# Kernel tuning notes

Measured on AMD Instinct MI355X. Metric: run time of the kernel, lower is better.

## Reference

```python
import jax, jax.numpy as jnp
import numpy as np
from jax.scipy.special import logsumexp

WORD_DIM = 512
SCRF_DIM = 256
N_TAGS = 12
ALLOWED_SPAN = 8
START_ID = 10
STOP_ID = 11
SEQ_LEN = 768
N_SPANS = 96


def _compute_scores(h, Wl, bl, Wr, br, Gl, bgl, Gr, bgr, Wt, bt, transitions):
    # h: [1, L, D] already projected by Dense
    Lc, D = h.shape[1], h.shape[2]
    scores = jnp.zeros((1, Lc, Lc, D), h.dtype)
    diag = jnp.arange(Lc)
    ht = h
    scores = scores.at[:, diag, diag].set(ht)
    for sl in range(1, min(ALLOWED_SPAN, Lc)):
        l, r = ht[:, :-1], ht[:, 1:]
        h_hat = 4.0 * jax.nn.sigmoid(l @ Wl.T + bl + r @ Wr.T + br) - 2.0
        # exp/normalize over 3 gates == softmax over gate axis
        g = (l @ Gl.T + bgl + r @ Gr.T + bgr).reshape(1, Lc - sl, 3, D)
        wgt = jax.nn.softmax(g, axis=2)
        ht = wgt[:, :, 0] * h_hat + wgt[:, :, 1] * l + wgt[:, :, 2] * r
        scores = scores.at[:, diag[:Lc - sl], diag[sl:]].set(ht)
    tagsc = scores @ Wt.T + bt  # [1, L, L, T]
    # final[b,i,j,prev,tag] = tagsc[b,i,j,tag] + transitions[prev,tag]
    return tagsc[:, :, :, None, :] + transitions[None, None, None]


def _forward_pass(s5):
    # s5: [1, L, L, T, T]; semi-Markov forward algorithm, windows of width <= ALLOWED_SPAN
    Lc, T = s5.shape[1], s5.shape[3]
    A = ALLOWED_SPAN
    i0 = jnp.arange(1, Lc + 1)
    k = jnp.arange(A)
    p = i0[:, None] - A + k[None, :]              # candidate span-start positions [L, A]
    m = p >= 0                                    # valid window mask (istarts = max(0, i-A))
    x = s5[0][jnp.clip(p, 0), (i0 - 1)[:, None]]  # [L, A, T, T] span scores ending at i-1
    buf0 = jnp.full((A, T), -10000.0, s5.dtype).at[A - 1, START_ID].set(0.0)

    def step(buf, inp):
        xi, mi = inp
        # tmp[k, prev, tag] = score + logalpha[start, prev]
        tmp = jnp.where(mi[:, None, None], xi + buf[:, :, None], -1e30)
        na = logsumexp(tmp, axis=(0, 1))  # [T]
        return jnp.concatenate([buf[1:], na[None]], axis=0), na

    _, alphas = jax.lax.scan(step, buf0, (x, m))
    return alphas[-1, :STOP_ID].sum()


def _gold_score(s5, tags):
    Lc, T = s5.shape[1], s5.shape[3]
    gf = tags[:, :, 0] * (Lc * T * T) + tags[:, :, 1] * (T * T) + tags[:, :, 2] * T + tags[:, :, 3]
    return jnp.take_along_axis(s5.reshape(1, -1), gf, axis=1).sum()


def setup_inputs() -> dict:
    key = jax.random.key(0)
    ks = jax.random.split(key, 16)
    D, W3 = SCRF_DIM, 3 * SCRF_DIM
    s = 0.05
    def w(k, shape):
        return jax.random.normal(k, shape, dtype=jnp.float32) * s
    return {
        "feats": jax.random.normal(ks[0], (1, SEQ_LEN, WORD_DIM), dtype=jnp.float32),
        "tags": jax.random.randint(ks[1], (1, N_SPANS, 4), 0, N_TAGS),
        "Wd": w(ks[2], (D, WORD_DIM)), "bd": jnp.zeros((D,), jnp.float32),
        "Wl": w(ks[3], (D, D)), "bl": jnp.zeros((D,), jnp.float32),
        "Wr": w(ks[4], (D, D)), "br": jnp.zeros((D,), jnp.float32),
        "Gl": w(ks[5], (W3, D)), "bgl": jnp.zeros((W3,), jnp.float32),
        "Gr": w(ks[6], (W3, D)), "bgr": jnp.zeros((W3,), jnp.float32),
        "Wt": w(ks[7], (N_TAGS, D)), "bt": jnp.zeros((N_TAGS,), jnp.float32),
        "transitions": w(ks[8], (N_TAGS, N_TAGS)),
    }


def reference(feats, tags, Wd, bd, Wl, bl, Wr, br, Gl, bgl, Gr, bgr, Wt, bt, transitions):
    h = feats @ Wd.T + bd  # Dense: word_dim -> scrf_dim
    s5 = _compute_scores(h, Wl, bl, Wr, br, Gl, bgl, Gr, bgr, Wt, bt, transitions)
    gold = _gold_score(s5, tags)
    logZ = _forward_pass(s5)
    return logZ - gold
```

## Files before the change

kernel.cpp:

```cpp
#include <hip/hip_runtime.h>

typedef __attribute__((ext_vector_type(8))) short short8;
typedef __attribute__((ext_vector_type(4))) float f32x4;

#define TPAD 100

__device__ __forceinline__ float bf2f(short s) {
  return __uint_as_float(((unsigned)(unsigned short)s) << 16);
}
__device__ __forceinline__ unsigned short f2bf(float f) {
  unsigned u = __float_as_uint(f);
  unsigned rounding = 0x7fffu + ((u >> 16) & 1u);
  return (unsigned short)((u + rounding) >> 16);
}

struct F8 { float4 a, b; };
__device__ __forceinline__ F8 ldf8(const float* p) {
  F8 r; r.a = *(const float4*)p; r.b = *(const float4*)(p + 4); return r;
}
__device__ __forceinline__ short8 cvtF8(F8 v) {
  short8 r;
  r[0]=(short)f2bf(v.a.x); r[1]=(short)f2bf(v.a.y); r[2]=(short)f2bf(v.a.z); r[3]=(short)f2bf(v.a.w);
  r[4]=(short)f2bf(v.b.x); r[5]=(short)f2bf(v.b.y); r[6]=(short)f2bf(v.b.z); r[7]=(short)f2bf(v.b.w);
  return r;
}

__device__ __forceinline__ void stg_f32(float* p, float v) {
  asm volatile("global_store_dword %0, %1, off sc1" :: "v"(p), "v"(v) : "memory");
}
__device__ __forceinline__ void stg_u16(unsigned short* p, unsigned short v) {
  unsigned w = v;
  asm volatile("global_store_short %0, %1, off sc1" :: "v"(p), "v"(w) : "memory");
}
__device__ __forceinline__ void stg_u32(unsigned* p, unsigned v) {
  asm volatile("global_store_dword %0, %1, off sc1" :: "v"(p), "v"(v) : "memory");
}

#define NFLAGS 30688
__device__ __forceinline__ void flag_spin(unsigned* f, unsigned tgt) {
  unsigned n = 0;
  while (__hip_atomic_load(f, __ATOMIC_RELAXED, __HIP_MEMORY_SCOPE_AGENT) < tgt) {
    __builtin_amdgcn_s_sleep(1);
    if (++n > 2000000u) break;
  }
}
#define DRAIN() asm volatile("s_waitcnt vmcnt(0) lgkmcnt(0)" ::: "memory")
#define KTBAR() do { \
  asm volatile("s_waitcnt lgkmcnt(0)" ::: "memory"); \
  __builtin_amdgcn_s_barrier(); \
  __builtin_amdgcn_sched_barrier(0); \
} while (0)

union __align__(16) SmemU {
  struct { unsigned short As[2][64][72]; unsigned short Ws[2][64][72]; float Cs[64][64]; } g;
  struct { unsigned short As8[8][64][72]; float Cs[64][64]; } gi;
  struct { unsigned short rows[8][264]; float sred[96]; float smu; } bn;
  struct { float Bs[96 * TPAD]; float Acs[96 * TPAD]; float red[8]; } t;
  struct { float Qs[2][96 * TPAD]; float vv[4][96]; float red[8]; float redm[4]; } f;
};

__global__ void prep_kernel(const float* __restrict__ bl, const float* __restrict__ br,
                            const float* __restrict__ bgl, const float* __restrict__ bgr,
                            float* __restrict__ bc, unsigned* __restrict__ flags)
{
  int idx = blockIdx.x * 256 + threadIdx.x;
  if (idx < 1024) {
    bc[idx] = (idx < 256) ? bl[idx] + br[idx] : bgl[idx-256] + bgr[idx-256];
  } else {
    int j = idx - 1024;
    if (j < NFLAGS) flags[j] = 0u;
  }
}

__device__ __forceinline__ void treelevel(SmemU& sm,
    const float* Tin, const float* Cin, float* Tout, float* Cout)
{
  const int bid = blockIdx.x;
  const int tid = threadIdx.x;
  const int wv = tid >> 6, lane = tid & 63;
  const int j = bid >> 1;
  const int cs = (bid & 1) * 48;
  const float* Ag = Tin + (size_t)(2*j) * 9216;
  const float* Bg = Tin + (size_t)(2*j + 1) * 9216;

  float4 av[9], bv[9];
  const float* ap = Ag + tid * 36;
  const float* bp = Bg + tid * 36;
  #pragma unroll
  for (int q = 0; q < 9; ++q) av[q] = *(const float4*)(ap + q*4);
  #pragma unroll
  for (int q = 0; q < 9; ++q) bv[q] = *(const float4*)(bp + q*4);
  float ma = 0.f, mb = 0.f;
  #pragma unroll
  for (int q = 0; q < 9; ++q) {
    ma = fmaxf(ma, fmaxf(fmaxf(av[q].x, av[q].y), fmaxf(av[q].z, av[q].w)));
    mb = fmaxf(mb, fmaxf(fmaxf(bv[q].x, bv[q].y), fmaxf(bv[q].z, bv[q].w)));
  }
  #pragma unroll
  for (int off = 32; off; off >>= 1) {
    ma = fmaxf(ma, __shfl_down(ma, off));
    mb = fmaxf(mb, __shfl_down(mb, off));
  }
  if (lane == 0) { sm.t.red[wv] = ma; sm.t.red[4 + wv] = mb; }
  __syncthreads();
  float fa = fmaxf(fmaxf(sm.t.red[0], sm.t.red[1]), fmaxf(sm.t.red[2], sm.t.red[3]));
  float fb = fmaxf(fmaxf(sm.t.red[4], sm.t.red[5]), fmaxf(sm.t.red[6], sm.t.red[7]));
  float ia = 1.0f / fa, ib = 1.0f / fb;

  #pragma unroll
  for (int q = 0; q < 9; ++q) {
    int e = tid*36 + q*4;
    int r = e / 96, k = e - r*96;
    float4 bb = bv[q];
    bb.x *= ib; bb.y *= ib; bb.z *= ib; bb.w *= ib;
    *(float4*)&sm.t.Bs[r*TPAD + k] = bb;
    float4 aa = av[q];
    sm.t.Acs[(k+0)*TPAD + r] = aa.x * ia;
    sm.t.Acs[(k+1)*TPAD + r] = aa.y * ia;
    sm.t.Acs[(k+2)*TPAD + r] = aa.z * ia;
    sm.t.Acs[(k+3)*TPAD + r] = aa.w * ia;
  }
  __syncthreads();

  int tr = tid >> 4, tc = tid & 15;
  int r0 = tr * 6, c0 = cs + tc * 3;
  float acc[6][3];
  #pragma unroll
  for (int i = 0; i < 6; ++i)
    #pragma unroll
    for (int m = 0; m < 3; ++m) acc[i][m] = 0.f;
  for (int k = 0; k < 96; k += 4) {
    float4 a0 = *(const float4*)&sm.t.Acs[(c0+0)*TPAD + k];
    float4 a1 = *(const float4*)&sm.t.Acs[(c0+1)*TPAD + k];
    float4 a2 = *(const float4*)&sm.t.Acs[(c0+2)*TPAD + k];
    #pragma unroll
    for (int i = 0; i < 6; ++i) {
      float4 b = *(const float4*)&sm.t.Bs[(r0+i)*TPAD + k];
      acc[i][0] += b.x*a0.x + b.y*a0.y + b.z*a0.z + b.w*a0.w;
      acc[i][1] += b.x*a1.x + b.y*a1.y + b.z*a1.z + b.w*a1.w;
      acc[i][2] += b.x*a2.x + b.y*a2.y + b.z*a2.z + b.w*a2.w;
    }
  }
  float* op = Tout + (size_t)j * 9216;
  #pragma unroll
  for (int i = 0; i < 6; ++i)
    #pragma unroll
    for (int m = 0; m < 3; ++m)
      stg_f32(&op[(size_t)(r0+i)*96 + c0 + m], acc[i][m]);
  if ((bid & 1) == 0 && tid == 0)
    stg_f32(&Cout[j], Cin[2*j] + Cin[2*j + 1] + __logf(fa) + __logf(fb));
}

__global__ __launch_bounds__(256, 1) void mega_kernel(
    const float* feats, const float* Wd, const float* bd,
    const float* Wl, const float* Wr, const float* Gl, const float* Gr,
    unsigned short* WcB, const float* bc,
    unsigned short* ht, const float* Wt, const float* bt,
    float* Bband, float* Xn, float* muv, const float* trans,
    const int* tags,
    float* T0, float* T1, float* T2, float* T3, float* T4,
    float* C0, float* C1, float* C2, float* C3, float* C4,
    float* out, unsigned* flags)
{
  __shared__ SmemU sm;
  const int bid = blockIdx.x;
  const int tid = threadIdx.x;
  const int wave = tid >> 6, lane = tid & 63;

  if (bid >= 48) {
    for (int j = (bid - 48)*256 + tid; j < 524288; j += 208*256) {
      int o = j >> 9, k = j & 511;
      float v;
      if (k < 256) v = (o < 256) ? Wl[o*256 + k] : Gl[(o-256)*256 + k];
      else { int k2 = k - 256; v = (o < 256) ? Wr[o*256 + k2] : Gr[(o-256)*256 + k2]; }
      stg_u16(&WcB[j], f2bf(v));
    }
    DRAIN();
    __syncthreads();
    if (tid == 0) atomicAdd(&flags[958*32], 1u);
  }

  if (bid < 192) {
    const int p = bid % 12;
    const int lr = tid >> 3;
    const int c8 = (tid & 7) * 8;
    const int q8 = (lane >> 4) * 8;
    if (bid < 48) {
      const int p0 = p * 64;
      const int n0 = (bid / 12) * 64;
      f32x4 acc[4];
      #pragma unroll
      for (int i = 0; i < 4; ++i)
        #pragma unroll
        for (int j = 0; j < 4; ++j) acc[i][j] = 0.f;
      F8 fa0[2], fa1[2], fw0[2], fw1[2];
      #pragma unroll
      for (int q = 0; q < 2; ++q) {
        int kb = q * 64;
        fa0[q] = ldf8(feats + (size_t)(p0 + lr)*512 + kb + c8);
        fa1[q] = ldf8(feats + (size_t)(p0 + lr + 32)*512 + kb + c8);
        fw0[q] = ldf8(Wd + (size_t)(n0 + lr)*512 + kb + c8);
        fw1[q] = ldf8(Wd + (size_t)(n0 + lr + 32)*512 + kb + c8);
      }
      #pragma unroll
      for (int kt = 0; kt < 8; ++kt) {
        const int sb = kt & 1;
        *(short8*)(&sm.g.As[sb][lr][c8])      = cvtF8(fa0[sb]);
        *(short8*)(&sm.g.As[sb][lr + 32][c8]) = cvtF8(fa1[sb]);
        *(short8*)(&sm.g.Ws[sb][lr][c8])      = cvtF8(fw0[sb]);
        *(short8*)(&sm.g.Ws[sb][lr + 32][c8]) = cvtF8(fw1[sb]);
        if (kt < 6) {
          int kb = (kt + 2) * 64;
          fa0[sb] = ldf8(feats + (size_t)(p0 + lr)*512 + kb + c8);
          fa1[sb] = ldf8(feats + (size_t)(p0 + lr + 32)*512 + kb + c8);
          fw0[sb] = ldf8(Wd + (size_t)(n0 + lr)*512 + kb + c8);
          fw1[sb] = ldf8(Wd + (size_t)(n0 + lr + 32)*512 + kb + c8);
        }
        KTBAR();
        #pragma unroll
        for (int kk = 0; kk < 2; ++kk) {
          short8 bfr = *(const short8*)(&sm.g.Ws[sb][wave*16 + (lane & 15)][kk*32 + q8]);
          #pragma unroll
          for (int mt = 0; mt < 4; ++mt) {
            short8 afr = *(const short8*)(&sm.g.As[sb][mt*16 + (lane & 15)][kk*32 + q8]);
            acc[mt] = __builtin_amdgcn_mfma_f32_16x16x32_bf16(afr, bfr, acc[mt], 0, 0, 0);
          }
        }
        KTBAR();
      }
      int o = n0 + wave*16 + (lane & 15);
      float bias = bd[o];
      #pragma unroll
      for (int mt = 0; mt < 4; ++mt)
        #pragma unroll
        for (int r = 0; r < 4; ++r) {
          int row = p0 + mt*16 + (lane >> 4)*4 + r;
          stg_u16(&ht[row*256 + o], f2bf(acc[mt][r] + bias));
        }
      DRAIN();
      __syncthreads();
      if (tid == 0) atomicAdd(&flags[(0*12 + p)*32], 1u);
    }

    const int p0 = p * 64;
    const int n0i = (bid / 12) * 16;
    if (tid == 0) flag_spin(&flags[958*32], 208u);
    __syncthreads();
    short8 wfrag[16];
    {
      const size_t wrow = (size_t)(wave*256 + n0i + (lane & 15)) * 512;
      #pragma unroll
      for (int kt = 0; kt < 8; ++kt)
        #pragma unroll
        for (int kk = 0; kk < 2; ++kk)
          wfrag[kt*2 + kk] = *(const short8*)(WcB + wrow + kt*64 + kk*32 + q8);
    }
    for (int sl = 1; sl <= 7; ++sl) {
      unsigned tgt = (sl == 1) ? 4u : 16u;
      if (tid == 0) flag_spin(&flags[((sl-1)*12 + p)*32], tgt);
      __syncthreads();
      const unsigned short* htp = ht + (size_t)(sl - 1) * 196608;
      unsigned short* htn = ht + (size_t)sl * 196608;
      const int Mvalid = 768 - sl;
      short8 areg[16];
      #pragma unroll
      for (int kt = 0; kt < 4; ++kt) {
        const int kcol = kt * 64;
        areg[kt*2]     = *(const short8*)(htp + (size_t)(p0 + lr)*256 + kcol + c8);
        areg[kt*2 + 1] = *(const short8*)(htp + (size_t)(p0 + lr + 32)*256 + kcol + c8);
      }
      if (tid == 64 && p < 11) flag_spin(&flags[((sl-1)*12 + p + 1)*32], tgt);
      #pragma unroll
      for (int kt = 0; kt < 4; ++kt) {
        *(short8*)(&sm.gi.As8[kt][lr][c8])      = areg[kt*2];
        *(short8*)(&sm.gi.As8[kt][lr + 32][c8]) = areg[kt*2 + 1];
      }
      __syncthreads();
      #pragma unroll
      for (int kt = 4; kt < 8; ++kt) {
        const int kcol = (kt & 3) * 64;
        int g0 = p0 + lr + 1;      if (g0 > 767) g0 = 767;
        int g1 = p0 + lr + 33;     if (g1 > 767) g1 = 767;
        areg[kt*2]     = *(const short8*)(htp + (size_t)g0*256 + kcol + c8);
        areg[kt*2 + 1] = *(const short8*)(htp + (size_t)g1*256 + kcol + c8);
      }
      #pragma unroll
      for (int kt = 4; kt < 8; ++kt) {
        *(short8*)(&sm.gi.As8[kt][lr][c8])      = areg[kt*2];
        *(short8*)(&sm.gi.As8[kt][lr + 32][c8]) = areg[kt*2 + 1];
      }
      __syncthreads();
      f32x4 acc[4];
      #pragma unroll
      for (int i = 0; i < 4; ++i)
        #pragma unroll
        for (int j = 0; j < 4; ++j) acc[i][j] = 0.f;
      #pragma unroll
      for (int kt = 0; kt < 8; ++kt) {
        #pragma unroll
        for (int kk = 0; kk < 2; ++kk) {
          #pragma unroll
          for (int mt = 0; mt < 4; ++mt) {
            short8 afr = *(const short8*)(&sm.gi.As8[kt][mt*16 + (lane & 15)][kk*32 + q8]);
            acc[mt] = __builtin_amdgcn_mfma_f32_16x16x32_bf16(afr, wfrag[kt*2 + kk], acc[mt], 0, 0, 0);
          }
        }
      }
      #pragma unroll
      for (int mt = 0; mt < 4; ++mt)
        #pragma unroll
        for (int r = 0; r < 4; ++r)
          sm.gi.Cs[mt*16 + (lane >> 4)*4 + r][wave*16 + (lane & 15)] = acc[mt][r];
      __syncthreads();

      {
        int dl = tid & 7;
        int d0 = n0i + dl*2;
        int cc0 = dl*2;
        float bz0 = bc[d0],       bz1 = bc[d0+1];
        float b00 = bc[256 + d0], b01 = bc[256 + d0 + 1];
        float b10 = bc[512 + d0], b11 = bc[512 + d0 + 1];
        float b20 = bc[768 + d0], b21 = bc[768 + d0 + 1];
        for (int pr = tid >> 3; pr < 64; pr += 32) {
          int pw = p0 + pr;
          if (pw >= Mvalid) continue;
          float z0 = sm.gi.Cs[pr][cc0]      + bz0, z1 = sm.gi.Cs[pr][cc0+1]      + bz1;
          float g00 = sm.gi.Cs[pr][16+cc0]  + b00, g01 = sm.gi.Cs[pr][16+cc0+1]  + b01;
          float g10 = sm.gi.Cs[pr][32+cc0]  + b10, g11 = sm.gi.Cs[pr][32+cc0+1]  + b11;
          float g20 = sm.gi.Cs[pr][48+cc0]  + b20, g21 = sm.gi.Cs[pr][48+cc0+1]  + b21;
          unsigned lv = *(const unsigned*)(htp + (size_t)pw*256 + d0);
          unsigned rv = *(const unsigned*)(htp + (size_t)(pw+1)*256 + d0);
          float l0 = bf2f((short)(lv & 0xffff)), l1 = bf2f((short)(lv >> 16));
          float r0v = bf2f((short)(rv & 0xffff)), r1v = bf2f((short)(rv >> 16));
          float hh0 = 4.f / (1.f + __expf(-z0)) - 2.f;
          float hh1 = 4.f / (1.f + __expf(-z1)) - 2.f;
          float mg0 = fmaxf(g00, fmaxf(g10, g20));
          float mg1 = fmaxf(g01, fmaxf(g11, g21));
          float e00 = __expf(g00 - mg0), e10 = __expf(g10 - mg0), e20 = __expf(g20 - mg0);
          float e01 = __expf(g01 - mg1), e11 = __expf(g11 - mg1), e21 = __expf(g21 - mg1);
          float o0 = (e00*hh0 + e10*l0 + e20*r0v) / (e00 + e10 + e20);
          float o1 = (e01*hh1 + e11*l1 + e21*r1v) / (e01 + e11 + e21);
          unsigned pack = (unsigned)f2bf(o0) | ((unsigned)f2bf(o1) << 16);
          stg_u32((unsigned*)(htn + (size_t)pw*256 + d0), pack);
        }
      }
      DRAIN();
      __syncthreads();
      if (tid == 0) atomicAdd(&flags[(sl*12 + p)*32], 1u);
    }
  }

  for (int i1 = bid; i1 < 768; i1 += 256) {
    const int i = i1 + 1;
    if (tid < 2) {
      int rlo = i - 8; if (rlo < 0) rlo = 0;
      int tlo = rlo >> 6, thi = (i - 1) >> 6;
      int tt = (tid == 0) ? tlo : thi;
      flag_spin(&flags[(7*12 + tt)*32], 16u);
    }
    __syncthreads();
    {
      int k = tid >> 5, cc = (tid & 31) * 8;
      int pr = i - 8 + k;
      short8 v;
      if (pr >= 0) {
        int slx = 7 - k;
        v = *(const short8*)(ht + ((size_t)slx*768 + pr)*256 + cc);
      } else {
        #pragma unroll
        for (int j = 0; j < 8; ++j) v[j] = 0;
      }
      *(short8*)(&sm.bn.rows[k][cc]) = v;
    }
    __syncthreads();
    float res = -1e30f;
    if (tid < 96) {
      int t = tid >> 3, k = tid & 7;
      int pr = i - 8 + k;
      if (pr >= 0) {
        float acc = 0.f;
        for (int dch = 0; dch < 256; dch += 8) {
          float4 wa = *(const float4*)(Wt + t*256 + dch);
          float4 wb = *(const float4*)(Wt + t*256 + dch + 4);
          short8 hv = *(const short8*)(&sm.bn.rows[k][dch]);
          acc += wa.x*bf2f(hv[0]) + wa.y*bf2f(hv[1]) + wa.z*bf2f(hv[2]) + wa.w*bf2f(hv[3])
               + wb.x*bf2f(hv[4]) + wb.y*bf2f(hv[5]) + wb.z*bf2f(hv[6]) + wb.w*bf2f(hv[7]);
        }
        res = acc + bt[t];
      }
      stg_f32(&Bband[(size_t)i*96 + tid], res);
      sm.bn.sred[tid] = res;
    }
    __syncthreads();
    if (tid < 32) {
      float m = fmaxf(sm.bn.sred[tid], fmaxf(sm.bn.sred[tid+32], sm.bn.sred[tid+64]));
      #pragma unroll
      for (int off = 16; off; off >>= 1) m = fmaxf(m, __shfl_down(m, off));
      if (tid == 0) { stg_f32(&muv[i], m); sm.bn.smu = m; }
    }
    __syncthreads();
    if (tid < 96) stg_f32(&Xn[(size_t)i*96 + tid], __expf(res - sm.bn.smu));
    DRAIN();
    __syncthreads();
    if (tid == 0) atomicAdd(&flags[(96 + i1)*32], 1u);
  }
  if (bid >= 240) return;

  {
    const int chunk = bid / 5;
    const int bxx = bid % 5;
    if (tid < 16) flag_spin(&flags[(96 + 16*chunk + tid)*32], 1u);
    __syncthreads();
    if (bxx == 0 && tid == 0) stg_f32(&C0[chunk], 0.f);
    const int a = chunk * 16;
    const int g = lane / 12;
    const int t = lane - g * 12;
    const int cidx = bxx * 20 + wave * 5 + g;
    const bool active = (g < 5) && (cidx < 96);
    const int c = active ? cidx : 95;
    const int s = c / 12, tau = c - s * 12;
    float Etc[12];
    #pragma unroll
    for (int jj = 0; jj < 12; ++jj) Etc[jj] = __expf(trans[jj*12 + t]);
    float NA[8], V[8];
    #pragma unroll
    for (int jj = 0; jj < 8; ++jj) { NA[jj] = 0.f; V[jj] = 0.f; }
    #pragma unroll
    for (int jj = 0; jj < 8; ++jj) if (jj == s) {
      NA[jj] = (t == tau) ? 1.f : 0.f;
      V[jj]  = Etc[tau];
    }
    const int gbb = (g * 12) * 4;
    #pragma unroll
    for (int m = 1; m <= 16; ++m) {
      const float* xr = Xn + (size_t)(a + m) * 96 + t * 8;
      float4 x0 = *(const float4*)xr;
      float4 x1 = *(const float4*)(xr + 4);
      float sf = __expf(-muv[a + m]);
      float na = x0.x*V[0] + x0.y*V[1] + x0.z*V[2] + x0.w*V[3]
               + x1.x*V[4] + x1.y*V[5] + x1.z*V[6] + x1.w*V[7];
      int nai = __float_as_int(na);
      float nb[12];
      #pragma unroll
      for (int jj = 0; jj < 12; ++jj)
        nb[jj] = __int_as_float(__builtin_amdgcn_ds_bpermute(gbb + jj*4, nai));
      float pp0 = nb[0]*Etc[0] + nb[1]*Etc[1] + nb[2]*Etc[2]   + nb[3]*Etc[3];
      float pp1 = nb[4]*Etc[4] + nb[5]*Etc[5] + nb[6]*Etc[6]   + nb[7]*Etc[7];
      float pp2 = nb[8]*Etc[8] + nb[9]*Etc[9] + nb[10]*Etc[10] + nb[11]*Etc[11];
      float v = (pp0 + pp1) + pp2;
      #pragma unroll
      for (int kq = 0; kq < 7; ++kq) { NA[kq] = NA[kq+1]*sf; V[kq] = V[kq+1]*sf; }
      NA[7] = na; V[7] = v;
    }
    if (active) {
      float* dst = T0 + (size_t)chunk * 9216 + c;
      #pragma unroll
      for (int jj = 0; jj < 8; ++jj) stg_f32(&dst[(size_t)(jj*12 + t) * 96], NA[jj]);
    }
    DRAIN();
    __syncthreads();
    if (tid == 0) atomicAdd(&flags[(864 + chunk)*32], 1u);
  }
  if (bid >= 48) return;

  {
    int j = bid >> 1;
    if (tid < 2) flag_spin(&flags[(864 + 2*j + tid)*32], 5u);
    __syncthreads();
    treelevel(sm, T0, C0, T1, C1);
    DRAIN(); __syncthreads();
    if (tid == 0) atomicAdd(&flags[(912 + j)*32], 1u);
  }
  if (bid >= 24) return;
  {
    int j = bid >> 1;
    if (tid < 2) flag_spin(&flags[(912 + 2*j + tid)*32], 2u);
    __syncthreads();
    treelevel(sm, T1, C1, T2, C2);
    DRAIN(); __syncthreads();
    if (tid == 0) atomicAdd(&flags[(936 + j)*32], 1u);
  }
  if (bid >= 12) return;
  {
    int j = bid >> 1;
    if (tid < 2) flag_spin(&flags[(936 + 2*j + tid)*32], 2u);
    __syncthreads();
    treelevel(sm, T2, C2, T3, C3);
    DRAIN(); __syncthreads();
    if (tid == 0) atomicAdd(&flags[(948 + j)*32], 1u);
  }
  if (bid >= 6) return;
  {
    int j = bid >> 1;
    if (tid < 2) flag_spin(&flags[(948 + 2*j + tid)*32], 2u);
    __syncthreads();
    treelevel(sm, T3, C3, T4, C4);
    DRAIN(); __syncthreads();
    if (tid == 0) atomicAdd(&flags[(954 + j)*32], 1u);
  }
  if (bid) return;

  {
    if (tid < 3) flag_spin(&flags[(954 + tid)*32], 2u);
    __syncthreads();
    float4 P[9];
    const float* p0p = T4 + tid * 36;
    #pragma unroll
    for (int q = 0; q < 9; ++q) P[q] = *(const float4*)(p0p + q*4);

    float gold = 0.f;
    if (tid < 96) {
      int a = tags[tid*4+0], b = tags[tid*4+1], cc = tags[tid*4+2], d = tags[tid*4+3];
      float v = trans[cc*12 + d];
      int sl = b - a;
      if (sl >= 0 && sl < 8) v += Bband[(size_t)(b+1)*96 + d*8 + (7 - sl)];
      else v += bt[d];
      gold = v;
    }
    float mp = 0.f;
    for (int q = tid; q < 768; q += 256) mp += muv[1 + q];
    #pragma unroll
    for (int off = 32; off; off >>= 1) {
      gold += __shfl_down(gold, off);
      mp   += __shfl_down(mp, off);
    }
    if (lane == 0) { sm.f.red[wave] = gold; sm.f.red[4 + wave] = mp; }

    #pragma unroll
    for (int q = 0; q < 9; ++q) {
      int e = tid*36 + q*4;
      int r = e / 96, k = e - r*96;
      *(float4*)&sm.f.Qs[0][r*TPAD + k] = P[q];
    }
    if (tid < 96) sm.f.vv[0][tid] = (tid == 94) ? 1.f : 0.f;
    __syncthreads();
    float gold_t = sm.f.red[0] + sm.f.red[1] + sm.f.red[2] + sm.f.red[3];
    float musum  = sm.f.red[4] + sm.f.red[5] + sm.f.red[6] + sm.f.red[7];
    float Ct = C4[0] + C4[1] + C4[2];

    #pragma unroll
    for (int s = 0; s < 3; ++s) {
      if (s < 2) {
        const float* pn = T4 + (size_t)(s+1)*9216 + tid*36;
        #pragma unroll
        for (int q = 0; q < 9; ++q) P[q] = *(const float4*)(pn + q*4);
      }
      float acc = 0.f;
      if (tid < 96) {
        const float* Qr = &sm.f.Qs[s & 1][tid * TPAD];
        #pragma unroll
        for (int k = 0; k < 96; k += 4) {
          float4 qv = *(const float4*)(Qr + k);
          float4 zv = *(const float4*)&sm.f.vv[s][k];
          acc += qv.x*zv.x + qv.y*zv.y + qv.z*zv.z + qv.w*zv.w;
        }
      }
      float am = (tid < 96) ? acc : 0.f;
      #pragma unroll
      for (int off = 32; off; off >>= 1) am = fmaxf(am, __shfl_down(am, off));
      if (lane == 0) sm.f.redm[wave] = am;
      __syncthreads();
      float mx = fmaxf(fmaxf(sm.f.redm[0], sm.f.redm[1]), fmaxf(sm.f.redm[2], sm.f.redm[3]));
      Ct += __logf(mx);
      if (tid < 96) sm.f.vv[s+1][tid] = acc / mx;
      if (s < 2) {
        #pragma unroll
        for (int q = 0; q < 9; ++q) {
          int e = tid*36 + q*4;
          int r = e / 96, k = e - r*96;
          *(float4*)&sm.f.Qs[(s+1)&1][r*TPAD + k] = P[q];
        }
      }
      __syncthreads();
    }
    if (tid == 0) {
      float lsum = 0.f;
      #pragma unroll
      for (int t = 0; t < 11; ++t) lsum += __logf(sm.f.vv[3][84 + t]);
      out[0] = lsum + 11.f * (Ct + musum) - gold_t;
    }
  }
}

extern "C" void kernel_launch(void* const* d_in, const int* in_sizes, int n_in,
                              void* d_out, int out_size, void* d_ws, size_t ws_size,
                              hipStream_t stream)
{
  const float* feats = (const float*)d_in[0];
  const int*   tags  = (const int*)  d_in[1];
  const float* Wd    = (const float*)d_in[2];
  const float* bd    = (const float*)d_in[3];
  const float* Wl    = (const float*)d_in[4];
  const float* bl    = (const float*)d_in[5];
  const float* Wr    = (const float*)d_in[6];
  const float* br    = (const float*)d_in[7];
  const float* Gl    = (const float*)d_in[8];
  const float* bgl   = (const float*)d_in[9];
  const float* Gr    = (const float*)d_in[10];
  const float* bgr   = (const float*)d_in[11];
  const float* Wt    = (const float*)d_in[12];
  const float* bt    = (const float*)d_in[13];
  const float* trans = (const float*)d_in[14];
  float* out = (float*)d_out;

  char* ws = (char*)d_ws;
  unsigned short* WcB    = (unsigned short*)(ws + 1048576);
  float*          bc     = (float*)         (ws + 2097152);
  unsigned short* ht     = (unsigned short*)(ws + 2101248);
  float*          Bband  = (float*)         (ws + 5246976);
  float*          Xn     = (float*)         (ws + 5542272);
  float*          muv    = (float*)         (ws + 5837568);
  float*          T0     = (float*)         (ws + 5841664);
  float*          T1     = (float*)         (ws + 7611136);
  float*          T2     = (float*)         (ws + 8495872);
  float*          T3     = (float*)         (ws + 8938240);
  float*          T4     = (float*)         (ws + 9159424);
  float*          C0     = (float*)         (ws + 9270016);
  float*          C1     = (float*)         (ws + 9270272);
  float*          C2     = (float*)         (ws + 9270528);
  float*          C3     = (float*)         (ws + 9270784);
  float*          C4     = (float*)         (ws + 9271040);
  unsigned*       flags  = (unsigned*)      (ws + 9271296);

  prep_kernel<<<124, 256, 0, stream>>>(bl, br, bgl, bgr, bc, flags);
  mega_kernel<<<256, 256, 0, stream>>>(feats, Wd, bd, Wl, Wr, Gl, Gr, WcB, bc,
                                       ht, Wt, bt, Bband, Xn, muv, trans, tags,
                                       T0, T1, T2, T3, T4, C0, C1, C2, C3, C4,
                                       out, flags);
}
```

Before: 193.0 us.

## Fuse tree reduction levels into radix-4 steps and drop bf16 weight prepass

The log-space matrix-product tree over forward-pass transfer matrices now combines four matrices per block per level instead of two, cutting the reduction from four flag-synchronised levels to two. Each block chains three 96x96 matmuls in shared memory with double-buffered partial products. Separately, the global bf16 conversion of the combined Wl/Wr/Gl/Gr weights, and the flag wait on it, is removed; each block now converts its own weight fragments from fp32 directly into registers. This trades extra serial matmul work per block, and redundant fp32 weight reads, for fewer grid-wide syncs and a shorter critical path.

```diff
diff --git a/kernel.cpp b/kernel.cpp
--- a/kernel.cpp
+++ b/kernel.cpp
@@ -55,7 +55,7 @@
   struct { unsigned short As[2][64][72]; unsigned short Ws[2][64][72]; float Cs[64][64]; } g;
   struct { unsigned short As8[8][64][72]; float Cs[64][64]; } gi;
   struct { unsigned short rows[8][264]; float sred[96]; float smu; } bn;
-  struct { float Bs[96 * TPAD]; float Acs[96 * TPAD]; float red[8]; } t;
+  struct { float Ms[96 * TPAD]; float Pc[2][96 * TPAD]; float red[8]; } t4;
   struct { float Qs[2][96 * TPAD]; float vv[4][96]; float red[8]; float redm[4]; } f;
 };
 
@@ -72,73 +72,83 @@
   }
 }
 
-__device__ __forceinline__ void treelevel(SmemU& sm,
-    const float* Tin, const float* Cin, float* Tout, float* Cout)
+__device__ __forceinline__ void tree4(SmemU& sm,
+    const float* Tin, const float* Cin, float* Tout, float* Cout, int j, int cs)
 {
-  const int bid = blockIdx.x;
   const int tid = threadIdx.x;
   const int wv = tid >> 6, lane = tid & 63;
-  const int j = bid >> 1;
-  const int cs = (bid & 1) * 48;
-  const float* Ag = Tin + (size_t)(2*j) * 9216;
-  const float* Bg = Tin + (size_t)(2*j + 1) * 9216;
-
-  float4 av[9], bv[9];
-  const float* ap = Ag + tid * 36;
-  const float* bp = Bg + tid * 36;
+  const int tr = tid >> 4, tc = tid & 15;
+  const int r0 = tr * 6, c0 = tc * 3;
+  float logsum = Cin[4*j] + Cin[4*j+1] + Cin[4*j+2] + Cin[4*j+3];
+  float acc[6][3];
+  int cur = 0;
   #pragma unroll
-  for (int q = 0; q < 9; ++q) av[q] = *(const float4*)(ap + q*4);
-  #pragma unroll
-  for (int q = 0; q < 9; ++q) bv[q] = *(const float4*)(bp + q*4);
-  float ma = 0.f, mb = 0.f;
-  #pragma unroll
-  for (int q = 0; q < 9; ++q) {
-    ma = fmaxf(ma, fmaxf(fmaxf(av[q].x, av[q].y), fmaxf(av[q].z, av[q].w)));
-    mb = fmaxf(mb, fmaxf(fmaxf(bv[q].x, bv[q].y), fmaxf(bv[q].z, bv[q].w)));
-  }
-  #pragma unroll
-  for (int off = 32; off; off >>= 1) {
-    ma = fmaxf(ma, __shfl_down(ma, off));
-    mb = fmaxf(mb, __shfl_down(mb, off));
-  }
-  if (lane == 0) { sm.t.red[wv] = ma; sm.t.red[4 + wv] = mb; }
-  __syncthreads();
-  float fa = fmaxf(fmaxf(sm.t.red[0], sm.t.red[1]), fmaxf(sm.t.red[2], sm.t.red[3]));
-  float fb = fmaxf(fmaxf(sm.t.red[4], sm.t.red[5]), fmaxf(sm.t.red[6], sm.t.red[7]));
-  float ia = 1.0f / fa, ib = 1.0f / fb;
-
-  #pragma unroll
-  for (int q = 0; q < 9; ++q) {
-    int e = tid*36 + q*4;
-    int r = e / 96, k = e - r*96;
-    float4 bb = bv[q];
-    bb.x *= ib; bb.y *= ib; bb.z *= ib; bb.w *= ib;
-    *(float4*)&sm.t.Bs[r*TPAD + k] = bb;
-    float4 aa = av[q];
-    sm.t.Acs[(k+0)*TPAD + r] = aa.x * ia;
-    sm.t.Acs[(k+1)*TPAD + r] = aa.y * ia;
-    sm.t.Acs[(k+2)*TPAD + r] = aa.z * ia;
-    sm.t.Acs[(k+3)*TPAD + r] = aa.w * ia;
-  }
-  __syncthreads();
-
-  int tr = tid >> 4, tc = tid & 15;
-  int r0 = tr * 6, c0 = cs + tc * 3;
-  float acc[6][3];
-  #pragma unroll
-  for (int i = 0; i < 6; ++i)
-    #pragma unroll
-    for (int m = 0; m < 3; ++m) acc[i][m] = 0.f;
-  for (int k = 0; k < 96; k += 4) {
-    float4 a0 = *(const float4*)&sm.t.Acs[(c0+0)*TPAD + k];
-    float4 a1 = *(const float4*)&sm.t.Acs[(c0+1)*TPAD + k];
-    float4 a2 = *(const float4*)&sm.t.Acs[(c0+2)*TPAD + k];
-    #pragma unroll
-    for (int i = 0; i < 6; ++i) {
-      float4 b = *(const float4*)&sm.t.Bs[(r0+i)*TPAD + k];
-      acc[i][0] += b.x*a0.x + b.y*a0.y + b.z*a0.z + b.w*a0.w;
-      acc[i][1] += b.x*a1.x + b.y*a1.y + b.z*a1.z + b.w*a1.w;
-      acc[i][2] += b.x*a2.x + b.y*a2.y + b.z*a2.z + b.w*a2.w;
+  for (int s = 0; s < 4; ++s) {
+    float4 mv[9];
+    const float* mp = Tin + (size_t)(4*j + s) * 9216 + tid*36;
+    #pragma unroll
+    for (int q = 0; q < 9; ++q) mv[q] = *(const float4*)(mp + q*4);
+    float mx = 0.f;
+    #pragma unroll
+    for (int q = 0; q < 9; ++q)
+      mx = fmaxf(mx, fmaxf(fmaxf(mv[q].x, mv[q].y), fmaxf(mv[q].z, mv[q].w)));
+    #pragma unroll
+    for (int off = 32; off; off >>= 1) mx = fmaxf(mx, __shfl_down(mx, off));
+    if (lane == 0) sm.t4.red[(s & 1)*4 + wv] = mx;
+    __syncthreads();
+    {
+      const float* rd = &sm.t4.red[(s & 1)*4];
+      mx = fmaxf(fmaxf(rd[0], rd[1]), fmaxf(rd[2], rd[3]));
+    }
+    float inv = 1.0f / mx;
+    logsum += __logf(mx);
+    if (s == 0) {
+      #pragma unroll
+      for (int q = 0; q < 9; ++q) {
+        int e = tid*36 + q*4;
+        int r = e / 96, k = e - r*96;
+        float vals[4] = {mv[q].x, mv[q].y, mv[q].z, mv[q].w};
+        #pragma unroll
+        for (int x = 0; x < 4; ++x) {
+          int cl = k + x - cs;
+          if ((unsigned)cl < 48u) sm.t4.Pc[0][cl*TPAD + r] = vals[x] * inv;
+        }
+      }
+      __syncthreads();
+    } else {
+      #pragma unroll
+      for (int q = 0; q < 9; ++q) {
+        int e = tid*36 + q*4;
+        int r = e / 96, k = e - r*96;
+        float4 m = mv[q];
+        m.x *= inv; m.y *= inv; m.z *= inv; m.w *= inv;
+        *(float4*)&sm.t4.Ms[r*TPAD + k] = m;
+      }
+      __syncthreads();
+      #pragma unroll
+      for (int i = 0; i < 6; ++i)
+        #pragma unroll
+        for (int m = 0; m < 3; ++m) acc[i][m] = 0.f;
+      for (int k = 0; k < 96; k += 4) {
+        float4 p0 = *(const float4*)&sm.t4.Pc[cur][(c0+0)*TPAD + k];
+        float4 p1 = *(const float4*)&sm.t4.Pc[cur][(c0+1)*TPAD + k];
+        float4 p2 = *(const float4*)&sm.t4.Pc[cur][(c0+2)*TPAD + k];
+        #pragma unroll
+        for (int i = 0; i < 6; ++i) {
+          float4 b = *(const float4*)&sm.t4.Ms[(r0+i)*TPAD + k];
+          acc[i][0] += b.x*p0.x + b.y*p0.y + b.z*p0.z + b.w*p0.w;
+          acc[i][1] += b.x*p1.x + b.y*p1.y + b.z*p1.z + b.w*p1.w;
+          acc[i][2] += b.x*p2.x + b.y*p2.y + b.z*p2.z + b.w*p2.w;
+        }
+      }
+      if (s < 3) {
+        #pragma unroll
+        for (int i = 0; i < 6; ++i)
+          #pragma unroll
+          for (int m = 0; m < 3; ++m)
+            sm.t4.Pc[cur ^ 1][(c0+m)*TPAD + (r0+i)] = acc[i][m];
+        cur ^= 1;
+      }
     }
   }
   float* op = Tout + (size_t)j * 9216;
@@ -146,39 +156,25 @@
   for (int i = 0; i < 6; ++i)
     #pragma unroll
     for (int m = 0; m < 3; ++m)
-      stg_f32(&op[(size_t)(r0+i)*96 + c0 + m], acc[i][m]);
-  if ((bid & 1) == 0 && tid == 0)
-    stg_f32(&Cout[j], Cin[2*j] + Cin[2*j + 1] + __logf(fa) + __logf(fb));
+      stg_f32(&op[(size_t)(r0+i)*96 + cs + c0 + m], acc[i][m]);
+  if (cs == 0 && tid == 0) stg_f32(&Cout[j], logsum);
 }
 
 __global__ __launch_bounds__(256, 1) void mega_kernel(
     const float* feats, const float* Wd, const float* bd,
     const float* Wl, const float* Wr, const float* Gl, const float* Gr,
-    unsigned short* WcB, const float* bc,
+    const float* bc,
     unsigned short* ht, const float* Wt, const float* bt,
     float* Bband, float* Xn, float* muv, const float* trans,
     const int* tags,
-    float* T0, float* T1, float* T2, float* T3, float* T4,
-    float* C0, float* C1, float* C2, float* C3, float* C4,
+    float* T0, float* T1, float* T2,
+    float* C0, float* C1, float* C2,
     float* out, unsigned* flags)
 {
   __shared__ SmemU sm;
   const int bid = blockIdx.x;
   const int tid = threadIdx.x;
   const int wave = tid >> 6, lane = tid & 63;
-
-  if (bid >= 48) {
-    for (int j = (bid - 48)*256 + tid; j < 524288; j += 208*256) {
-      int o = j >> 9, k = j & 511;
-      float v;
-      if (k < 256) v = (o < 256) ? Wl[o*256 + k] : Gl[(o-256)*256 + k];
-      else { int k2 = k - 256; v = (o < 256) ? Wr[o*256 + k2] : Gr[(o-256)*256 + k2]; }
-      stg_u16(&WcB[j], f2bf(v));
-    }
-    DRAIN();
-    __syncthreads();
-    if (tid == 0) atomicAdd(&flags[958*32], 1u);
-  }
 
   if (bid < 192) {
     const int p = bid % 12;
@@ -244,16 +240,21 @@
 
     const int p0 = p * 64;
     const int n0i = (bid / 12) * 16;
-    if (tid == 0) flag_spin(&flags[958*32], 208u);
-    __syncthreads();
     short8 wfrag[16];
     {
-      const size_t wrow = (size_t)(wave*256 + n0i + (lane & 15)) * 512;
-      #pragma unroll
-      for (int kt = 0; kt < 8; ++kt)
+      const int o = wave*256 + n0i + (lane & 15);
+      const float* b0 = (o < 256) ? (Wl + (size_t)o*256) : (Gl + (size_t)(o-256)*256);
+      const float* b1 = (o < 256) ? (Wr + (size_t)o*256) : (Gr + (size_t)(o-256)*256);
+      #pragma unroll
+      for (int kt = 0; kt < 4; ++kt)
         #pragma unroll
         for (int kk = 0; kk < 2; ++kk)
-          wfrag[kt*2 + kk] = *(const short8*)(WcB + wrow + kt*64 + kk*32 + q8);
+          wfrag[kt*2 + kk] = cvtF8(ldf8(b0 + kt*64 + kk*32 + q8));
+      #pragma unroll
+      for (int kt = 4; kt < 8; ++kt)
+        #pragma unroll
+        for (int kk = 0; kk < 2; ++kk)
+          wfrag[kt*2 + kk] = cvtF8(ldf8(b1 + (kt-4)*64 + kk*32 + q8));
     }
     for (int sl = 1; sl <= 7; ++sl) {
       unsigned tgt = (sl == 1) ? 4u : 16u;
@@ -461,50 +462,32 @@
     __syncthreads();
     if (tid == 0) atomicAdd(&flags[(864 + chunk)*32], 1u);
   }
-  if (bid >= 48) return;
+  if (bid >= 24) return;
 
   {
-    int j = bid >> 1;
-    if (tid < 2) flag_spin(&flags[(864 + 2*j + tid)*32], 5u);
-    __syncthreads();
-    treelevel(sm, T0, C0, T1, C1);
+    int j = bid >> 1, cs = (bid & 1) * 48;
+    if (tid < 4) flag_spin(&flags[(864 + 4*j + tid)*32], 5u);
+    __syncthreads();
+    tree4(sm, T0, C0, T1, C1, j, cs);
     DRAIN(); __syncthreads();
     if (tid == 0) atomicAdd(&flags[(912 + j)*32], 1u);
   }
-  if (bid >= 24) return;
-  {
-    int j = bid >> 1;
-    if (tid < 2) flag_spin(&flags[(912 + 2*j + tid)*32], 2u);
-    __syncthreads();
-    treelevel(sm, T1, C1, T2, C2);
-    DRAIN(); __syncthreads();
-    if (tid == 0) atomicAdd(&flags[(936 + j)*32], 1u);
-  }
-  if (bid >= 12) return;
-  {
-    int j = bid >> 1;
-    if (tid < 2) flag_spin(&flags[(936 + 2*j + tid)*32], 2u);
-    __syncthreads();
-    treelevel(sm, T2, C2, T3, C3);
-    DRAIN(); __syncthreads();
-    if (tid == 0) atomicAdd(&flags[(948 + j)*32], 1u);
-  }
   if (bid >= 6) return;
   {
-    int j = bid >> 1;
-    if (tid < 2) flag_spin(&flags[(948 + 2*j + tid)*32], 2u);
-    __syncthreads();
-    treelevel(sm, T3, C3, T4, C4);
+    int j = bid >> 1, cs = (bid & 1) * 48;
+    if (tid < 4) flag_spin(&flags[(912 + 4*j + tid)*32], 2u);
+    __syncthreads();
+    tree4(sm, T1, C1, T2, C2, j, cs);
     DRAIN(); __syncthreads();
-    if (tid == 0) atomicAdd(&flags[(954 + j)*32], 1u);
+    if (tid == 0) atomicAdd(&flags[(928 + j)*32], 1u);
   }
   if (bid) return;
 
   {
-    if (tid < 3) flag_spin(&flags[(954 + tid)*32], 2u);
+    if (tid < 3) flag_spin(&flags[(928 + tid)*32], 2u);
     __syncthreads();
     float4 P[9];
-    const float* p0p = T4 + tid * 36;
+    const float* p0p = T2 + tid * 36;
     #pragma unroll
     for (int q = 0; q < 9; ++q) P[q] = *(const float4*)(p0p + q*4);
 
@@ -536,12 +519,12 @@
     __syncthreads();
     float gold_t = sm.f.red[0] + sm.f.red[1] + sm.f.red[2] + sm.f.red[3];
     float musum  = sm.f.red[4] + sm.f.red[5] + sm.f.red[6] + sm.f.red[7];
-    float Ct = C4[0] + C4[1] + C4[2];
+    float Ct = C2[0] + C2[1] + C2[2];
 
     #pragma unroll
     for (int s = 0; s < 3; ++s) {
       if (s < 2) {
-        const float* pn = T4 + (size_t)(s+1)*9216 + tid*36;
+        const float* pn = T2 + (size_t)(s+1)*9216 + tid*36;
         #pragma unroll
         for (int q = 0; q < 9; ++q) P[q] = *(const float4*)(pn + q*4);
       }
@@ -604,7 +587,6 @@
   float* out = (float*)d_out;
 
   char* ws = (char*)d_ws;
-  unsigned short* WcB    = (unsigned short*)(ws + 1048576);
   float*          bc     = (float*)         (ws + 2097152);
   unsigned short* ht     = (unsigned short*)(ws + 2101248);
   float*          Bband  = (float*)         (ws + 5246976);
@@ -613,18 +595,14 @@
   float*          T0     = (float*)         (ws + 5841664);
   float*          T1     = (float*)         (ws + 7611136);
   float*          T2     = (float*)         (ws + 8495872);
-  float*          T3     = (float*)         (ws + 8938240);
-  float*          T4     = (float*)         (ws + 9159424);
   float*          C0     = (float*)         (ws + 9270016);
   float*          C1     = (float*)         (ws + 9270272);
   float*          C2     = (float*)         (ws + 9270528);
-  float*          C3     = (float*)         (ws + 9270784);
-  float*          C4     = (float*)         (ws + 9271040);
   unsigned*       flags  = (unsigned*)      (ws + 9271296);
 
   prep_kernel<<<124, 256, 0, stream>>>(bl, br, bgl, bgr, bc, flags);
-  mega_kernel<<<256, 256, 0, stream>>>(feats, Wd, bd, Wl, Wr, Gl, Gr, WcB, bc,
+  mega_kernel<<<256, 256, 0, stream>>>(feats, Wd, bd, Wl, Wr, Gl, Gr, bc,
                                        ht, Wt, bt, Bband, Xn, muv, trans, tags,
-                                       T0, T1, T2, T3, T4, C0, C1, C2, C3, C4,
+                                       T0, T1, T2, C0, C1, C2,
                                        out, flags);
 }
```

Result: no change. 194.2 us (+0.7%).
